# Kernel tuning notes

Measured on AMD Instinct MI355X. Metric: run time of the kernel, lower is better.

Reference implementation:

```python
import jax, jax.numpy as jnp
import numpy as np

NUM_HEADS = 12
D_MODEL = 768


def setup_inputs() -> dict:
    key = jax.random.key(0)
    ks = jax.random.split(key, 5)
    B, S = 2, 2048
    x = jax.random.normal(ks[0], (B, S, D_MODEL), dtype=jnp.float32)
    # additive causal mask: 0 on/below diagonal, -1e9 above
    causal = jnp.tril(jnp.ones((S, S), dtype=bool))
    attn_mask = jnp.where(causal, 0.0, -1e9).astype(jnp.float32)
    lim_in = 1.0 / np.sqrt(D_MODEL)
    w_in = jax.random.uniform(ks[1], (3 * D_MODEL, D_MODEL), jnp.float32, -lim_in, lim_in)
    b_in = jax.random.uniform(ks[2], (3 * D_MODEL,), jnp.float32, -lim_in, lim_in)
    w_out = jax.random.uniform(ks[3], (D_MODEL, D_MODEL), jnp.float32, -lim_in, lim_in)
    b_out = jax.random.uniform(ks[4], (D_MODEL,), jnp.float32, -lim_in, lim_in)
    return {"x": x, "attn_mask": attn_mask, "w_in": w_in, "b_in": b_in,
            "w_out": w_out, "b_out": b_out}


def reference(x, attn_mask, w_in, b_in, w_out, b_out):
    B, S, d_model = x.shape
    H = NUM_HEADS
    d_head = d_model // H
    # fused QKV projection (torch Linear: x @ W^T + b)
    projected = x @ w_in.T + b_in                      # [B, S, 3*d_model]
    # faithful reinterpretation as in the source: row-major view to
    # [B*H, S, d_head, 3] (q/k/v interleaved on last axis, heads folded
    # across the flat buffer). No 1/sqrt(d_head) scaling in the source.
    qkv = projected.reshape(B * H, S, d_head, 3)
    q = qkv[..., 0]                                    # [B*H, S, d_head]
    k = qkv[..., 1]
    v = qkv[..., 2]
    logits = jnp.einsum('nsd,ntd->nst', q, k) + attn_mask  # [B*H, S, S]
    weights = jax.nn.softmax(logits, axis=-1)          # dropout_p = 0
    heads = jnp.einsum('nst,ntd->nsd', weights, v)     # [B*H, S, d_head]
    out = heads.reshape(B, H, S, d_head).transpose(0, 2, 1, 3).reshape(B, S, d_model)
    return out @ w_out.T + b_out
```

## Files before the change

### kernel.cpp

```cpp
#include <hip/hip_runtime.h>
#include <hip/hip_bf16.h>
#include <stdint.h>

typedef __attribute__((ext_vector_type(8))) short bf16x8;
typedef __attribute__((ext_vector_type(4))) float f32x4;
typedef __attribute__((ext_vector_type(16))) float f32x16;
typedef __attribute__((ext_vector_type(4))) unsigned short u16x4;

__device__ __forceinline__ unsigned short f2bf(float f) {
    unsigned int u = __builtin_bit_cast(unsigned int, f);
    u = (u + 0x7fffu + ((u >> 16) & 1u)) >> 16;
    return (unsigned short)u;
}

__device__ __forceinline__ float bf2f(unsigned short u) {
    unsigned int x = ((unsigned int)u) << 16;
    return __builtin_bit_cast(float, x);
}

__device__ __forceinline__ void gl2lds16(const void* g, void* l) {
    __builtin_amdgcn_global_load_lds(
        (const __attribute__((address_space(1))) unsigned int*)g,
        (__attribute__((address_space(3))) unsigned int*)l, 16, 0, 0);
}

__global__ __launch_bounds__(256)
void cvt_all(const float* __restrict__ x, const float* __restrict__ wi, const float* __restrict__ wo,
             unsigned short* __restrict__ xb, unsigned short* __restrict__ wb1,
             unsigned short* __restrict__ wb2) {
    const int bid = blockIdx.x;
    const float* src; unsigned short* dst; int i;
    if (bid < 3072)      { src = x;  dst = xb;  i = bid * 256 + threadIdx.x; }
    else if (bid < 4800) { src = wi; dst = wb1; i = (bid - 3072) * 256 + threadIdx.x; }
    else                 { src = wo; dst = wb2; i = (bid - 4800) * 256 + threadIdx.x; }
    float4 v = reinterpret_cast<const float4*>(src)[i];
    union { unsigned short u[4]; uint2 p; } o;
    o.u[0] = f2bf(v.x); o.u[1] = f2bf(v.y); o.u[2] = f2bf(v.z); o.u[3] = f2bf(v.w);
    reinterpret_cast<uint2*>(dst)[i] = o.p;
}

template<int BM, int BN>
__global__ __launch_bounds__(256)
void gemm_bt(const unsigned short* __restrict__ A, const unsigned short* __restrict__ B,
             const float* __restrict__ bias, int M, int N, int K, int mode,
             unsigned short* __restrict__ bf_out, float* __restrict__ f32_out) {
    __shared__ unsigned short Al[2][BM][32];
    __shared__ unsigned short Bl[2][BN][32];
    const int tid = threadIdx.x;
    const int wid = tid >> 6, lane = tid & 63;
    const int m0 = blockIdx.y * BM, n0 = blockIdx.x * BN;
    const int wm = (wid >> 1) * (BM / 2), wn = (wid & 1) * (BN / 2);
    const int lrow = lane & 15;
    constexpr int MR = BM / 32, NR = BN / 32;
    f32x4 acc[MR][NR];
#pragma unroll
    for (int a = 0; a < MR; a++)
#pragma unroll
        for (int b = 0; b < NR; b++) acc[a][b] = f32x4{0.f, 0.f, 0.f, 0.f};

    auto stage = [&](int buf, int k0) {
#pragma unroll
        for (int i = 0; i < BM / 64; i++) {
            const int fb = i * 256 + tid;
            const int row = fb >> 2, blk = fb & 3;
            const int sb = blk ^ ((row >> 1) & 3);
            gl2lds16(&A[(size_t)(m0 + row) * K + k0 + sb * 8],
                     (char*)&Al[buf][0][0] + (i * 256 + (tid & ~63)) * 16);
        }
#pragma unroll
        for (int i = 0; i < BN / 64; i++) {
            const int fb = i * 256 + tid;
            const int row = fb >> 2, blk = fb & 3;
            const int sb = blk ^ ((row >> 1) & 3);
            gl2lds16(&B[(size_t)(n0 + row) * K + k0 + sb * 8],
                     (char*)&Bl[buf][0][0] + (i * 256 + (tid & ~63)) * 16);
        }
    };

    stage(0, 0);
    const int NS = K >> 5;
    for (int it = 0; it < NS; ++it) {
        __syncthreads();
        const int cur = it & 1;
        if (it + 1 < NS) stage(cur ^ 1, (it + 1) << 5);
        bf16x8 af[MR], bfr[NR];
#pragma unroll
        for (int i = 0; i < MR; i++) {
            const int row = wm + i * 16 + lrow;
            const int g = (lane >> 4) ^ ((row >> 1) & 3);
            af[i] = *reinterpret_cast<const bf16x8*>(&Al[cur][row][g * 8]);
        }
#pragma unroll
        for (int i = 0; i < NR; i++) {
            const int row = wn + i * 16 + lrow;
            const int g = (lane >> 4) ^ ((row >> 1) & 3);
            bfr[i] = *reinterpret_cast<const bf16x8*>(&Bl[cur][row][g * 8]);
        }
#pragma unroll
        for (int mi = 0; mi < MR; mi++)
#pragma unroll
            for (int ni = 0; ni < NR; ni++)
                acc[mi][ni] = __builtin_amdgcn_mfma_f32_16x16x32_bf16(af[mi], bfr[ni], acc[mi][ni], 0, 0, 0);
    }
    const int rb = (lane >> 4) * 4;
#pragma unroll
    for (int mi = 0; mi < MR; mi++)
#pragma unroll
        for (int ni = 0; ni < NR; ni++) {
            int cc = n0 + wn + ni * 16 + lrow;
            float bv = bias[cc];
#pragma unroll
            for (int i = 0; i < 4; i++) {
                int r = m0 + wm + mi * 16 + rb + i;
                float v = acc[mi][ni][i] + bv;
                if (mode == 0) {
                    bf_out[(size_t)r * N + cc] = f2bf(v);
                } else {
                    f32_out[(size_t)r * N + cc] = v;
                }
            }
        }
}

__global__ __launch_bounds__(256)
void deint(const unsigned short* __restrict__ P, unsigned short* __restrict__ qkv) {
    __shared__ unsigned short L[6144];
    const int tid = threadIdx.x;
    const size_t base = (size_t)blockIdx.x * 6144;
#pragma unroll
    for (int s = 0; s < 3; ++s) {
        int idx = (s * 256 + tid) * 8;
        *reinterpret_cast<bf16x8*>(&L[idx]) = *reinterpret_cast<const bf16x8*>(&P[base + idx]);
    }
    __syncthreads();
    const int u0 = blockIdx.x * 32;
    const int n = u0 >> 11, t0 = u0 & 2047;
#pragma unroll
    for (int s = 0; s < 2; ++s) {
        int ww = s * 256 + tid;
        int j = ww >> 8;
        int cc = (ww & 255) >> 3;
        int o = ww & 7;
        bf16x8 vv;
#pragma unroll
        for (int q = 0; q < 8; ++q) vv[q] = (short)L[cc * 192 + 3 * (o * 8 + q) + j];
        *reinterpret_cast<bf16x8*>(&qkv[(size_t)j * 3145728 + (size_t)(u0 + cc) * 64 + o * 8]) = vv;
    }
    {
        int d = tid >> 2, g = tid & 3;
        bf16x8 vv;
#pragma unroll
        for (int e = 0; e < 8; ++e) vv[e] = (short)L[(g * 8 + e) * 192 + 3 * d + 2];
        *reinterpret_cast<bf16x8*>(&qkv[6291456 + (size_t)n * 131072 + (size_t)d * 2048 + t0 + g * 8]) = vv;
    }
}

__global__ __launch_bounds__(256, 4)
void attn_fwd(const unsigned short* __restrict__ qkv, unsigned short* __restrict__ Hb,
              unsigned short* __restrict__ Op, float2* __restrict__ Ml) {
    __shared__ unsigned short Kl[2][64][64];
    __shared__ unsigned short Vl[2][64][64];
    static const unsigned char CLS[40] = {
        60,61,62,63, 56,57,58, 52,53,54, 48,49,50, 44,45,46, 40,41, 36,37,
        32,33, 28,29, 24, 20, 16, 12, 59,42,25,8, 55,38,21,4, 51,34,17,0};
    const int tid = threadIdx.x, w = tid >> 6, lane = tid & 63;
    const int l31 = lane & 31, l7 = lane & 7, hi = lane >> 5;

    const int item = blockIdx.x;
    const int c = item / 24;
    const int n = item - c * 24;
    const int v = CLS[c];
    const int qb = v >> 2, ch = v & 3;
    const int ntfull = 2 * qb + 2;
    const int nch = (ntfull + 7) >> 3;
    const int split = (nch > 1) ? 1 : 0;
    const int tstart = ch * 8;
    const int nt = (ntfull - tstart < 8) ? (ntfull - tstart) : 8;
    const int q0w = qb * 128 + w * 32;
    const int q_lane = q0w + l31;
    const unsigned short* Qg = qkv + (size_t)n * 131072;
    const unsigned short* Kg = qkv + 3145728 + (size_t)n * 131072;
    const unsigned short* Vg = qkv + 6291456 + (size_t)n * 131072;

    bf16x8 qf[4];
#pragma unroll
    for (int s = 0; s < 4; s++)
        qf[s] = *reinterpret_cast<const bf16x8*>(&Qg[(size_t)q_lane * 64 + 16*s + 8*hi]);

    f32x16 oa[2];
#pragma unroll
    for (int dt = 0; dt < 2; dt++)
#pragma unroll
        for (int r = 0; r < 16; r++) oa[dt][r] = 0.f;
    float m_run = -3.0e38f, l_run = 0.f;

    auto stage = [&](int buf, int gt) {
        const int tb = gt * 64;
#pragma unroll
        for (int i = 0; i < 2; i++) {
            const int fb_base = i * 256 + (tid & ~63);
            const int fb = i * 256 + tid;
            const int t = fb >> 3, p = fb & 7;
            gl2lds16(&Kg[(size_t)(tb + t) * 64 + ((p ^ (t & 7)) << 3)],
                     (char*)&Kl[buf][0][0] + fb_base * 16);
            gl2lds16(&Vg[(size_t)t * 2048 + tb + ((p ^ (t & 7)) << 3)],
                     (char*)&Vl[buf][0][0] + fb_base * 16);
        }
    };

    stage(0, tstart);
    int cur = 0;
    for (int tt = 0; tt < nt; ++tt) {
        __syncthreads();
        const int t0 = (tstart + tt) * 64;
        if (tt + 1 < nt) stage(cur ^ 1, tstart + tt + 1);
        if (t0 <= q0w + 31) {
            f32x16 sa[2];
#pragma unroll
            for (int t2 = 0; t2 < 2; t2++)
#pragma unroll
                for (int r = 0; r < 16; r++) sa[t2][r] = 0.f;
            __builtin_amdgcn_s_setprio(1);
#pragma unroll
            for (int t2 = 0; t2 < 2; t2++)
#pragma unroll
                for (int s = 0; s < 4; s++) {
                    bf16x8 kf = *reinterpret_cast<const bf16x8*>(
                        &Kl[cur][32*t2 + l31][((2*s + hi) ^ l7) << 3]);
                    sa[t2] = __builtin_amdgcn_mfma_f32_32x32x16_bf16(kf, qf[s], sa[t2], 0, 0, 0);
                }
            __builtin_amdgcn_s_setprio(0);
            if (t0 + 63 > q0w) {
#pragma unroll
                for (int t2 = 0; t2 < 2; t2++)
#pragma unroll
                    for (int r = 0; r < 16; r++) {
                        int t = t0 + 32*t2 + (r & 3) + 8*(r >> 2) + 4*hi;
                        if (t > q_lane) sa[t2][r] = -1e30f;
                    }
            }
            float pm = sa[0][0];
#pragma unroll
            for (int t2 = 0; t2 < 2; t2++)
#pragma unroll
                for (int r = 0; r < 16; r++) pm = fmaxf(pm, sa[t2][r]);
            pm = fmaxf(pm, __shfl_xor(pm, 32));
            if (__any(pm > m_run + 8.f)) {
                float mn = fmaxf(m_run, pm);
                float alpha = __expf(m_run - mn);
                l_run *= alpha;
#pragma unroll
                for (int dt = 0; dt < 2; dt++)
#pragma unroll
                    for (int r = 0; r < 16; r++) oa[dt][r] *= alpha;
                m_run = mn;
            }
            float rs = 0.f;
#pragma unroll
            for (int t2 = 0; t2 < 2; t2++)
#pragma unroll
                for (int r = 0; r < 16; r++) {
                    float p = __expf(sa[t2][r] - m_run);
                    sa[t2][r] = p;
                    rs += p;
                }
            rs += __shfl_xor(rs, 32);
            l_run += rs;
            bf16x8 pfrag[4];
#pragma unroll
            for (int t2 = 0; t2 < 2; t2++) {
                unsigned int pk[8];
#pragma unroll
                for (int k2 = 0; k2 < 8; k2++) {
                    float lo = sa[t2][2*k2], hi2 = sa[t2][2*k2 + 1];
                    unsigned int r;
                    asm("v_cvt_pk_bf16_f32 %0, %1, %2" : "=v"(r) : "v"(lo), "v"(hi2));
                    pk[k2] = r;
                }
                asm("v_permlane32_swap_b32 %0, %1" : "+v"(pk[0]), "+v"(pk[2]));
                asm("v_permlane32_swap_b32 %0, %1" : "+v"(pk[1]), "+v"(pk[3]));
                asm("v_permlane32_swap_b32 %0, %1" : "+v"(pk[4]), "+v"(pk[6]));
                asm("v_permlane32_swap_b32 %0, %1" : "+v"(pk[5]), "+v"(pk[7]));
                union { unsigned int u[4]; bf16x8 v; } f0, f1;
                f0.u[0] = pk[0]; f0.u[1] = pk[1]; f0.u[2] = pk[2]; f0.u[3] = pk[3];
                f1.u[0] = pk[4]; f1.u[1] = pk[5]; f1.u[2] = pk[6]; f1.u[3] = pk[7];
                pfrag[2*t2]     = f0.v;
                pfrag[2*t2 + 1] = f1.v;
            }
            __builtin_amdgcn_s_setprio(1);
#pragma unroll
            for (int dt = 0; dt < 2; dt++)
#pragma unroll
                for (int sp = 0; sp < 4; sp++) {
                    bf16x8 vf = *reinterpret_cast<const bf16x8*>(
                        &Vl[cur][32*dt + l31][((2*sp + hi) ^ l7) << 3]);
                    oa[dt] = __builtin_amdgcn_mfma_f32_32x32x16_bf16(vf, pfrag[sp], oa[dt], 0, 0, 0);
                }
            __builtin_amdgcn_s_setprio(0);
        }
        cur ^= 1;
    }
    const int b = n / 12, h = n - (n / 12) * 12;
    if (!split) {
        const float inv = 1.0f / l_run;
        const size_t rowb = ((size_t)(b * 2048 + q_lane)) * 768 + h * 64;
#pragma unroll
        for (int dt = 0; dt < 2; dt++)
#pragma unroll
            for (int g = 0; g < 4; g++) {
                u16x4 o4;
#pragma unroll
                for (int e = 0; e < 4; e++) o4[e] = f2bf(oa[dt][4*g + e] * inv);
                *reinterpret_cast<u16x4*>(&Hb[rowb + 32*dt + 8*g + 4*hi]) = o4;
            }
    } else {
        const int rr = q_lane - 512;
        const size_t pbase = ((size_t)(n * 1536 + rr) * 4 + ch) * 64;
#pragma unroll
        for (int dt = 0; dt < 2; dt++)
#pragma unroll
            for (int g = 0; g < 4; g++) {
                u16x4 o4;
#pragma unroll
                for (int e = 0; e < 4; e++) o4[e] = f2bf(oa[dt][4*g + e]);
                *reinterpret_cast<u16x4*>(&Op[pbase + 32*dt + 8*g + 4*hi]) = o4;
            }
        if (hi == 0) {
            float2 mlv; mlv.x = m_run; mlv.y = l_run;
            Ml[(n * 1536 + rr) * 4 + ch] = mlv;
        }
    }
}

__global__ __launch_bounds__(256)
void attn_combine(const unsigned short* __restrict__ Op, const float2* __restrict__ Ml,
                  unsigned short* __restrict__ Hb) {
    const int idx = blockIdx.x * 256 + threadIdx.x;
    const int d = idx & 63, rowg = idx >> 6;
    const int n = rowg / 1536, rr = rowg - n * 1536;
    const int qb = (512 + rr) >> 7;
    const int nch = (2 * qb + 9) >> 3;
    float M = -3.0e38f;
    for (int c = 0; c < nch; c++) M = fmaxf(M, Ml[rowg * 4 + c].x);
    float lsum = 0.f, osum = 0.f;
    for (int c = 0; c < nch; c++) {
        const float2 ml = Ml[rowg * 4 + c];
        const float wgt = __expf(ml.x - M);
        lsum += wgt * ml.y;
        osum += wgt * bf2f(Op[(size_t)(rowg * 4 + c) * 64 + d]);
    }
    const int bb = n / 12, h = n - (n / 12) * 12;
    Hb[((size_t)(bb * 2048 + 512 + rr)) * 768 + h * 64 + d] = f2bf(osum / lsum);
}

extern "C" void kernel_launch(void* const* d_in, const int* in_sizes, int n_in,
                              void* d_out, int out_size, void* d_ws, size_t ws_size,
                              hipStream_t stream) {
    const float* x     = (const float*)d_in[0];
    const float* w_in  = (const float*)d_in[2];
    const float* b_in  = (const float*)d_in[3];
    const float* w_out = (const float*)d_in[4];
    const float* b_out = (const float*)d_in[5];
    float* out = (float*)d_out;

    unsigned short* xb   = (unsigned short*)d_ws;
    unsigned short* wb1  = xb  + 3145728;
    unsigned short* wb2  = wb1 + 1769472;
    unsigned short* proj = wb2 + 589824;
    unsigned short* qkvb = proj + 9437184;
    unsigned short* hb   = qkvb + 9437184;
    unsigned short* Opb  = hb + 3145728;
    float2*       Ml  = (float2*)(Opb + 9437184);

    cvt_all<<<5376, 256, 0, stream>>>(x, w_in, w_out, xb, wb1, wb2);

    gemm_bt<128,128><<<dim3(18, 32), 256, 0, stream>>>(
        xb, wb1, b_in, 4096, 2304, 768, 0, proj, nullptr);

    deint<<<1536, 256, 0, stream>>>(proj, qkvb);

    attn_fwd<<<960, 256, 0, stream>>>(qkvb, hb, Opb, Ml);

    attn_combine<<<9216, 256, 0, stream>>>(Opb, Ml, hb);

    gemm_bt<128,64><<<dim3(12, 32), 256, 0, stream>>>(
        hb, wb2, b_out, 4096, 768, 768, 1, nullptr, out);
}
```

Baseline: 173.2 us.

## Split attention KV range into 4-tile chunks and stage tiles through registers

The causal KV range per query block is split into chunks of 4 tiles instead of 8, giving 72 work items per head (1728 blocks) and a larger split-combine pass. K/V tile staging moves from async global-to-LDS double buffering to register prefetch followed by an LDS store and an extra barrier, with single-buffered LDS. The aim is finer load balance and lower LDS use per block for higher occupancy. The cost is more partial outputs to write and combine, plus an extra sync per tile.

```diff
diff --git a/kernel.cpp b/kernel.cpp
--- a/kernel.cpp
+++ b/kernel.cpp
@@ -158,11 +158,14 @@
 __global__ __launch_bounds__(256, 4)
 void attn_fwd(const unsigned short* __restrict__ qkv, unsigned short* __restrict__ Hb,
               unsigned short* __restrict__ Op, float2* __restrict__ Ml) {
-    __shared__ unsigned short Kl[2][64][64];
-    __shared__ unsigned short Vl[2][64][64];
-    static const unsigned char CLS[40] = {
-        60,61,62,63, 56,57,58, 52,53,54, 48,49,50, 44,45,46, 40,41, 36,37,
-        32,33, 28,29, 24, 20, 16, 12, 59,42,25,8, 55,38,21,4, 51,34,17,0};
+    __shared__ unsigned short Kl[64][64];
+    __shared__ unsigned short Vl[64][64];
+    static const unsigned char CLS[72] = {
+        120,121,122,123,124,125,126,127, 112,113,114,115,116,117,118,
+        104,105,106,107,108,109,110, 96,97,98,99,100,101, 88,89,90,91,92,93,
+        80,81,82,83,84, 72,73,74,75,76, 64,65,66,67, 56,57,58,59,
+        48,49,50, 40,41,42, 32,33, 24,25, 16, 8,
+        119,102,85,68,51,34,17,0};
     const int tid = threadIdx.x, w = tid >> 6, lane = tid & 63;
     const int l31 = lane & 31, l7 = lane & 7, hi = lane >> 5;
 
@@ -170,12 +173,11 @@
     const int c = item / 24;
     const int n = item - c * 24;
     const int v = CLS[c];
-    const int qb = v >> 2, ch = v & 3;
+    const int qb = v >> 3, ch = v & 7;
     const int ntfull = 2 * qb + 2;
-    const int nch = (ntfull + 7) >> 3;
-    const int split = (nch > 1) ? 1 : 0;
-    const int tstart = ch * 8;
-    const int nt = (ntfull - tstart < 8) ? (ntfull - tstart) : 8;
+    const int split = (ntfull > 4) ? 1 : 0;
+    const int tstart = ch * 4;
+    const int nt = (ntfull - tstart < 4) ? (ntfull - tstart) : 4;
     const int q0w = qb * 128 + w * 32;
     const int q_lane = q0w + l31;
     const unsigned short* Qg = qkv + (size_t)n * 131072;
@@ -194,26 +196,30 @@
         for (int r = 0; r < 16; r++) oa[dt][r] = 0.f;
     float m_run = -3.0e38f, l_run = 0.f;
 
-    auto stage = [&](int buf, int gt) {
+    bf16x8 kreg[2], vreg[2];
+    auto loadtile = [&](int gt) {
         const int tb = gt * 64;
 #pragma unroll
         for (int i = 0; i < 2; i++) {
-            const int fb_base = i * 256 + (tid & ~63);
             const int fb = i * 256 + tid;
             const int t = fb >> 3, p = fb & 7;
-            gl2lds16(&Kg[(size_t)(tb + t) * 64 + ((p ^ (t & 7)) << 3)],
-                     (char*)&Kl[buf][0][0] + fb_base * 16);
-            gl2lds16(&Vg[(size_t)t * 2048 + tb + ((p ^ (t & 7)) << 3)],
-                     (char*)&Vl[buf][0][0] + fb_base * 16);
+            kreg[i] = *reinterpret_cast<const bf16x8*>(&Kg[(size_t)(tb + t) * 64 + ((p ^ (t & 7)) << 3)]);
+            vreg[i] = *reinterpret_cast<const bf16x8*>(&Vg[(size_t)t * 2048 + tb + ((p ^ (t & 7)) << 3)]);
         }
     };
 
-    stage(0, tstart);
-    int cur = 0;
+    loadtile(tstart);
     for (int tt = 0; tt < nt; ++tt) {
         __syncthreads();
+#pragma unroll
+        for (int i = 0; i < 2; i++) {
+            const int fb = i * 256 + tid;
+            *reinterpret_cast<bf16x8*>((char*)&Kl[0][0] + fb * 16) = kreg[i];
+            *reinterpret_cast<bf16x8*>((char*)&Vl[0][0] + fb * 16) = vreg[i];
+        }
+        __syncthreads();
         const int t0 = (tstart + tt) * 64;
-        if (tt + 1 < nt) stage(cur ^ 1, tstart + tt + 1);
+        if (tt + 1 < nt) loadtile(tstart + tt + 1);
         if (t0 <= q0w + 31) {
             f32x16 sa[2];
 #pragma unroll
@@ -226,7 +232,7 @@
 #pragma unroll
                 for (int s = 0; s < 4; s++) {
                     bf16x8 kf = *reinterpret_cast<const bf16x8*>(
-                        &Kl[cur][32*t2 + l31][((2*s + hi) ^ l7) << 3]);
+                        &Kl[32*t2 + l31][((2*s + hi) ^ l7) << 3]);
                     sa[t2] = __builtin_amdgcn_mfma_f32_32x32x16_bf16(kf, qf[s], sa[t2], 0, 0, 0);
                 }
             __builtin_amdgcn_s_setprio(0);
@@ -293,12 +299,11 @@
 #pragma unroll
                 for (int sp = 0; sp < 4; sp++) {
                     bf16x8 vf = *reinterpret_cast<const bf16x8*>(
-                        &Vl[cur][32*dt + l31][((2*sp + hi) ^ l7) << 3]);
+                        &Vl[32*dt + l31][((2*sp + hi) ^ l7) << 3]);
                     oa[dt] = __builtin_amdgcn_mfma_f32_32x32x16_bf16(vf, pfrag[sp], oa[dt], 0, 0, 0);
                 }
             __builtin_amdgcn_s_setprio(0);
         }
-        cur ^= 1;
     }
     const int b = n / 12, h = n - (n / 12) * 12;
     if (!split) {
@@ -314,8 +319,8 @@
                 *reinterpret_cast<u16x4*>(&Hb[rowb + 32*dt + 8*g + 4*hi]) = o4;
             }
     } else {
-        const int rr = q_lane - 512;
-        const size_t pbase = ((size_t)(n * 1536 + rr) * 4 + ch) * 64;
+        const int rr = q_lane - 256;
+        const size_t pbase = ((size_t)(n * 1792 + rr) * 8 + ch) * 64;
 #pragma unroll
         for (int dt = 0; dt < 2; dt++)
 #pragma unroll
@@ -327,7 +332,7 @@
             }
         if (hi == 0) {
             float2 mlv; mlv.x = m_run; mlv.y = l_run;
-            Ml[(n * 1536 + rr) * 4 + ch] = mlv;
+            Ml[(n * 1792 + rr) * 8 + ch] = mlv;
         }
     }
 }
@@ -337,20 +342,20 @@
                   unsigned short* __restrict__ Hb) {
     const int idx = blockIdx.x * 256 + threadIdx.x;
     const int d = idx & 63, rowg = idx >> 6;
-    const int n = rowg / 1536, rr = rowg - n * 1536;
-    const int qb = (512 + rr) >> 7;
-    const int nch = (2 * qb + 9) >> 3;
+    const int n = rowg / 1792, rr = rowg - n * 1792;
+    const int qb = (256 + rr) >> 7;
+    const int nch = (2 * qb + 5) >> 2;
     float M = -3.0e38f;
-    for (int c = 0; c < nch; c++) M = fmaxf(M, Ml[rowg * 4 + c].x);
+    for (int c = 0; c < nch; c++) M = fmaxf(M, Ml[rowg * 8 + c].x);
     float lsum = 0.f, osum = 0.f;
     for (int c = 0; c < nch; c++) {
-        const float2 ml = Ml[rowg * 4 + c];
+        const float2 ml = Ml[rowg * 8 + c];
         const float wgt = __expf(ml.x - M);
         lsum += wgt * ml.y;
-        osum += wgt * bf2f(Op[(size_t)(rowg * 4 + c) * 64 + d]);
+        osum += wgt * bf2f(Op[(size_t)(rowg * 8 + c) * 64 + d]);
     }
     const int bb = n / 12, h = n - (n / 12) * 12;
-    Hb[((size_t)(bb * 2048 + 512 + rr)) * 768 + h * 64 + d] = f2bf(osum / lsum);
+    Hb[((size_t)(bb * 2048 + 256 + rr)) * 768 + h * 64 + d] = f2bf(osum / lsum);
 }
 
 extern "C" void kernel_launch(void* const* d_in, const int* in_sizes, int n_in,
@@ -370,7 +375,7 @@
     unsigned short* qkvb = proj + 9437184;
     unsigned short* hb   = qkvb + 9437184;
     unsigned short* Opb  = hb + 3145728;
-    float2*       Ml  = (float2*)(Opb + 9437184);
+    float2*       Ml  = (float2*)(Opb + 22020096);
 
     cvt_all<<<5376, 256, 0, stream>>>(x, w_in, w_out, xb, wb1, wb2);
 
@@ -379,9 +384,9 @@
 
     deint<<<1536, 256, 0, stream>>>(proj, qkvb);
 
-    attn_fwd<<<960, 256, 0, stream>>>(qkvb, hb, Opb, Ml);
-
-    attn_combine<<<9216, 256, 0, stream>>>(Opb, Ml, hb);
+    attn_fwd<<<1728, 256, 0, stream>>>(qkvb, hb, Opb, Ml);
+
+    attn_combine<<<10752, 256, 0, stream>>>(Opb, Ml, hb);
 
     gemm_bt<128,64><<<dim3(12, 32), 256, 0, stream>>>(
         hb, wb2, b_out, 4096, 768, 768, 1, nullptr, out);
```

New measurement: 192.8 us. 1.11x slower.
